# Kernel optimization log

Measured on AMD Instinct MI355X. Metric: run time of the kernel, lower is better.

## Reference

```python
import jax, jax.numpy as jnp
import numpy as np

B, H, W, C = 4, 64, 64, 512
D = C // 8  # query/key channels

def setup_inputs() -> dict:
    key = jax.random.key(0)
    k1, k2, k3, k4, k5 = jax.random.split(key, 5)
    x = jax.random.normal(k1, (B, H, W, C), dtype=jnp.float32)
    # 1x1 convs without bias == per-pixel matmuls; he_normal-ish scaling
    Wq = jax.random.normal(k2, (C, D), dtype=jnp.float32) * np.sqrt(2.0 / C)
    Wk = jax.random.normal(k3, (C, D), dtype=jnp.float32) * np.sqrt(2.0 / C)
    Wv = jax.random.normal(k4, (C, C), dtype=jnp.float32) * np.sqrt(2.0 / C)
    # original init is zeros; use small nonzero so the attention path is exercised
    gamma = jax.random.normal(k5, (1,), dtype=jnp.float32) * 0.1
    return {"x": x, "Wq": Wq, "Wk": Wk, "Wv": Wv, "gamma": gamma}

def reference(x, Wq, Wk, Wv, gamma):
    b, h, w, c = x.shape
    n = h * w
    xf = x.reshape(b, n, c)                      # flatten spatial dims
    q = xf @ Wq                                  # [b, n, c//8]
    k = xf @ Wk                                  # [b, n, c//8]
    v = xf @ Wv                                  # [b, n, c]
    scores = jnp.einsum('bnd,bmd->bnm', q, k)    # [b, n, n]
    attn = jax.nn.sigmoid(scores)                # activation_func='sigmoid' (no row normalization)
    attended = jnp.einsum('bnm,bmc->bnc', attn, v).reshape(b, h, w, c)
    return gamma * attended + x
```

## Files before the change

kernel.cpp:

```cpp
#include <hip/hip_runtime.h>

typedef short bf16x8 __attribute__((ext_vector_type(8)));
typedef float f32x4 __attribute__((ext_vector_type(4)));
typedef unsigned short ushort8v __attribute__((ext_vector_type(8)));
typedef unsigned short ushort4v __attribute__((ext_vector_type(4)));

__device__ __forceinline__ unsigned short f2bf(float f) {
  unsigned u = __float_as_uint(f);
  u += 0x7FFF + ((u >> 16) & 1);
  return (unsigned short)(u >> 16);
}

__global__ void wt_prep(const float* __restrict__ Wq, const float* __restrict__ Wk,
                        const float* __restrict__ Wv, unsigned short* __restrict__ WbT) {
  int idx = blockIdx.x * 256 + threadIdx.x;
  int o = idx >> 9, c = idx & 511;
  float v;
  if (o < 64)       v = Wq[c * 64 + o] * 1.44269504f;
  else if (o < 128) v = Wk[c * 64 + (o - 64)];
  else              v = Wv[(size_t)c * 512 + (o - 128)];
  WbT[idx] = f2bf(v);
}

__global__ __launch_bounds__(256, 2) void proj_gemm(
    const float* __restrict__ x, const unsigned short* __restrict__ WbT,
    unsigned short* __restrict__ q, unsigned short* __restrict__ k,
    unsigned short* __restrict__ vT) {
  __shared__ unsigned short As[128][72];
  const int tid = threadIdx.x;
  const int wid = tid >> 6, lane = tid & 63;
  const int l15 = lane & 15, l4 = lane >> 4;
  const int mtile = blockIdx.x, ntile = blockIdx.y;
  const int rbase = mtile * 128;
  const int wr = (wid >> 1) * 64, wc = (wid & 1) * 64;

  f32x4 acc[4][4] = {};

  const int arow = tid >> 2;
  const int akof = (tid & 3) * 16;

  for (int kb = 0; kb < 512; kb += 64) {
    f32x4 t0[2][4];
#pragma unroll
    for (int pass = 0; pass < 2; ++pass) {
      const float* src = x + (size_t)(rbase + pass * 64 + arow) * 512 + kb + akof;
#pragma unroll
      for (int i = 0; i < 4; ++i) t0[pass][i] = *(const f32x4*)(src + i * 4);
    }
    __syncthreads();
#pragma unroll
    for (int pass = 0; pass < 2; ++pass) {
      unsigned short tmp[16];
#pragma unroll
      for (int i = 0; i < 4; ++i)
#pragma unroll
        for (int j = 0; j < 4; ++j) tmp[i * 4 + j] = f2bf(t0[pass][i][j]);
      unsigned short* dst = &As[pass * 64 + arow][akof];
      *(ushort8v*)(dst)     = *(ushort8v*)(tmp);
      *(ushort8v*)(dst + 8) = *(ushort8v*)(tmp + 8);
    }
    __syncthreads();

    bf16x8 af[4][2], bfr[4][2];
#pragma unroll
    for (int mr = 0; mr < 4; ++mr)
#pragma unroll
      for (int ks = 0; ks < 2; ++ks)
        af[mr][ks] = *(const bf16x8*)&As[wr + mr * 16 + l15][ks * 32 + l4 * 8];
#pragma unroll
    for (int nc = 0; nc < 4; ++nc)
#pragma unroll
      for (int ks = 0; ks < 2; ++ks) {
        int col = ntile * 128 + wc + nc * 16 + l15;
        bfr[nc][ks] = *(const bf16x8*)(WbT + (size_t)col * 512 + kb + ks * 32 + l4 * 8);
      }
#pragma unroll
    for (int ks = 0; ks < 2; ++ks)
#pragma unroll
      for (int mr = 0; mr < 4; ++mr)
#pragma unroll
        for (int nc = 0; nc < 4; ++nc)
          acc[mr][nc] = __builtin_amdgcn_mfma_f32_16x16x32_bf16(af[mr][ks], bfr[nc][ks],
                                                                acc[mr][nc], 0, 0, 0);
  }

  if (ntile == 0) {
    unsigned short* dst = (wid & 1) ? k : q;
#pragma unroll
    for (int mr = 0; mr < 4; ++mr)
#pragma unroll
      for (int nc = 0; nc < 4; ++nc)
#pragma unroll
        for (int r = 0; r < 4; ++r) {
          int grow = rbase + wr + mr * 16 + l4 * 4 + r;
          int col = nc * 16 + l15;
          dst[(size_t)grow * 64 + col] = f2bf(acc[mr][nc][r]);
        }
  } else {
#pragma unroll
    for (int mr = 0; mr < 4; ++mr)
#pragma unroll
      for (int nc = 0; nc < 4; ++nc) {
        int col = ntile * 128 + wc + nc * 16 + l15 - 128;
        int grow = rbase + wr + mr * 16 + l4 * 4;
        int b = grow >> 12, m = grow & 4095;
        ushort4v pk;
#pragma unroll
        for (int r = 0; r < 4; ++r) pk[r] = f2bf(acc[mr][nc][r]);
        *(ushort4v*)(vT + ((size_t)b * 512 + col) * 4096 + m) = pk;
      }
  }
}

__global__ __launch_bounds__(512, 2) void attn_fused(
    const float* __restrict__ x, const unsigned short* __restrict__ q,
    const unsigned short* __restrict__ k, const unsigned short* __restrict__ vT,
    const float* __restrict__ gamma, float* __restrict__ out) {
  __shared__ unsigned short Ks[64][72];
  __shared__ unsigned short Vs[256][72];
  __shared__ unsigned short Ps[128][72];
  const int tid = threadIdx.x, w = tid >> 6, lane = tid & 63;
  const int l15 = lane & 15, l4 = lane >> 4;
  const int rhalf = w >> 2;
  const int mt = w & 3;
  const int rt = blockIdx.x, ct = blockIdx.y, b = blockIdx.z;
  const int rbase = rt * 128, cbase = ct * 256;
  const unsigned short* qb = q + (size_t)b * 4096 * 64;
  const unsigned short* kp = k + (size_t)b * 4096 * 64;
  const unsigned short* vb = vT + (size_t)b * 512 * 4096;
  const float gv = gamma[0];

  const int kst_m = tid >> 3, kst_d = (tid & 7) * 8;
  const int vst_c = tid >> 1, vst_h = (tid & 1) * 32;

  bf16x8 qf[4][2];
#pragma unroll
  for (int rf = 0; rf < 4; ++rf)
#pragma unroll
    for (int ks = 0; ks < 2; ++ks)
      qf[rf][ks] = *(const bf16x8*)(qb +
          (size_t)(rbase + rhalf * 64 + rf * 16 + l15) * 64 + ks * 32 + l4 * 8);

  {
    bf16x8 kreg = *(const bf16x8*)(kp + (size_t)kst_m * 64 + kst_d);
    bf16x8 vreg[4];
#pragma unroll
    for (int i = 0; i < 4; ++i)
      vreg[i] = *(const bf16x8*)(vb + (size_t)(cbase + vst_c) * 4096 + vst_h + i * 8);
    *(bf16x8*)&Ks[kst_m][kst_d] = kreg;
#pragma unroll
    for (int i = 0; i < 4; ++i) *(bf16x8*)&Vs[vst_c][vst_h + i * 8] = vreg[i];
  }
  __syncthreads();

  f32x4 oacc[4][4] = {};

  for (int it = 0; it < 64; ++it) {
    const int mb_n = (it + 1) * 64;
    const bool pf = (it < 63);
    bf16x8 kreg; bf16x8 vreg[4];
    if (pf) {
      kreg = *(const bf16x8*)(kp + (size_t)(mb_n + kst_m) * 64 + kst_d);
#pragma unroll
      for (int i = 0; i < 4; ++i)
        vreg[i] = *(const bf16x8*)(vb + (size_t)(cbase + vst_c) * 4096 + mb_n + vst_h + i * 8);
    }

    f32x4 sacc[4] = {};
#pragma unroll
    for (int ks = 0; ks < 2; ++ks) {
      bf16x8 kf = *(const bf16x8*)&Ks[mt * 16 + l15][ks * 32 + l4 * 8];
#pragma unroll
      for (int rf = 0; rf < 4; ++rf)
        sacc[rf] = __builtin_amdgcn_mfma_f32_16x16x32_bf16(kf, qf[rf][ks], sacc[rf], 0, 0, 0);
    }
#pragma unroll
    for (int rf = 0; rf < 4; ++rf) {
      ushort4v pk;
#pragma unroll
      for (int r = 0; r < 4; ++r) {
        float s = sacc[rf][r];
        pk[r] = f2bf(__builtin_amdgcn_rcpf(1.0f + __builtin_amdgcn_exp2f(-s)));
      }
      *(ushort4v*)&Ps[rhalf * 64 + rf * 16 + l15][mt * 16 + l4 * 4] = pk;
    }
    __syncthreads();

    if (pf) *(bf16x8*)&Ks[kst_m][kst_d] = kreg;

#pragma unroll
    for (int kk = 0; kk < 2; ++kk) {
      bf16x8 af[4], bfr[4];
#pragma unroll
      for (int mr = 0; mr < 4; ++mr)
        af[mr] = *(const bf16x8*)&Ps[rhalf * 64 + mr * 16 + l15][kk * 32 + l4 * 8];
#pragma unroll
      for (int nc = 0; nc < 4; ++nc)
        bfr[nc] = *(const bf16x8*)&Vs[mt * 64 + nc * 16 + l15][kk * 32 + l4 * 8];
#pragma unroll
      for (int mr = 0; mr < 4; ++mr)
#pragma unroll
        for (int nc = 0; nc < 4; ++nc)
          oacc[mr][nc] = __builtin_amdgcn_mfma_f32_16x16x32_bf16(af[mr], bfr[nc],
                                                                 oacc[mr][nc], 0, 0, 0);
    }
    __syncthreads();

    if (pf) {
#pragma unroll
      for (int i = 0; i < 4; ++i) *(bf16x8*)&Vs[vst_c][vst_h + i * 8] = vreg[i];
    }
  }

#pragma unroll
  for (int mr = 0; mr < 4; ++mr)
#pragma unroll
    for (int nc = 0; nc < 4; ++nc)
#pragma unroll
      for (int r = 0; r < 4; ++r) {
        int grow = rbase + rhalf * 64 + mr * 16 + l4 * 4 + r;
        int col = cbase + mt * 64 + nc * 16 + l15;
        size_t idx = ((size_t)b * 4096 + grow) * 512 + col;
        out[idx] = gv * oacc[mr][nc][r] + x[idx];
      }
}

extern "C" void kernel_launch(void* const* d_in, const int* in_sizes, int n_in,
                              void* d_out, int out_size, void* d_ws, size_t ws_size,
                              hipStream_t stream) {
  const float* x     = (const float*)d_in[0];
  const float* Wq    = (const float*)d_in[1];
  const float* Wk    = (const float*)d_in[2];
  const float* Wv    = (const float*)d_in[3];
  const float* gamma = (const float*)d_in[4];
  float* out = (float*)d_out;

  char* ws = (char*)d_ws;
  unsigned short* qbuf = (unsigned short*)(ws);
  unsigned short* kbuf = (unsigned short*)(ws + (2ull << 20));
  unsigned short* vT   = (unsigned short*)(ws + (4ull << 20));
  unsigned short* WbT  = (unsigned short*)(ws + (20ull << 20));

  hipLaunchKernelGGL(wt_prep, dim3(1280), dim3(256), 0, stream, Wq, Wk, Wv, WbT);
  hipLaunchKernelGGL(proj_gemm, dim3(128, 5), dim3(256), 0, stream, x, WbT, qbuf, kbuf, vT);
  hipLaunchKernelGGL(attn_fused, dim3(32, 2, 4), dim3(512), 0, stream,
                     x, qbuf, kbuf, vT, gamma, out);
}
```

Baseline: 162.0 us.

## Shrink attention tile to 64 rows with 256-thread blocks and MFMA priority hints

The attention kernel now processes 64 query rows per block with 4 waves instead of 128 rows with 8 waves, doubling the grid to 512 blocks and redistributing the K/V staging loads per thread. The aim is more blocks for better CU occupancy and load balance. The cost is that each staged K/V tile is reused by half as many rows, which doubles global K/V traffic. s_setprio is also raised around the MFMA sections so matrix work gets issue priority over other waves.

```diff
diff --git a/kernel.cpp b/kernel.cpp
--- a/kernel.cpp
+++ b/kernel.cpp
@@ -112,26 +112,24 @@
   }
 }
 
-__global__ __launch_bounds__(512, 2) void attn_fused(
+__global__ __launch_bounds__(256, 2) void attn_fused(
     const float* __restrict__ x, const unsigned short* __restrict__ q,
     const unsigned short* __restrict__ k, const unsigned short* __restrict__ vT,
     const float* __restrict__ gamma, float* __restrict__ out) {
   __shared__ unsigned short Ks[64][72];
   __shared__ unsigned short Vs[256][72];
-  __shared__ unsigned short Ps[128][72];
+  __shared__ unsigned short Ps[64][72];
   const int tid = threadIdx.x, w = tid >> 6, lane = tid & 63;
   const int l15 = lane & 15, l4 = lane >> 4;
-  const int rhalf = w >> 2;
-  const int mt = w & 3;
   const int rt = blockIdx.x, ct = blockIdx.y, b = blockIdx.z;
-  const int rbase = rt * 128, cbase = ct * 256;
+  const int rbase = rt * 64, cbase = ct * 256;
   const unsigned short* qb = q + (size_t)b * 4096 * 64;
   const unsigned short* kp = k + (size_t)b * 4096 * 64;
   const unsigned short* vb = vT + (size_t)b * 512 * 4096;
   const float gv = gamma[0];
 
-  const int kst_m = tid >> 3, kst_d = (tid & 7) * 8;
-  const int vst_c = tid >> 1, vst_h = (tid & 1) * 32;
+  const int kst_m = tid >> 2, kst_d = (tid & 3) * 16;
+  const int vst_c = tid;
 
   bf16x8 qf[4][2];
 #pragma unroll
@@ -139,17 +137,19 @@
 #pragma unroll
     for (int ks = 0; ks < 2; ++ks)
       qf[rf][ks] = *(const bf16x8*)(qb +
-          (size_t)(rbase + rhalf * 64 + rf * 16 + l15) * 64 + ks * 32 + l4 * 8);
+          (size_t)(rbase + rf * 16 + l15) * 64 + ks * 32 + l4 * 8);
 
   {
-    bf16x8 kreg = *(const bf16x8*)(kp + (size_t)kst_m * 64 + kst_d);
-    bf16x8 vreg[4];
-#pragma unroll
-    for (int i = 0; i < 4; ++i)
-      vreg[i] = *(const bf16x8*)(vb + (size_t)(cbase + vst_c) * 4096 + vst_h + i * 8);
-    *(bf16x8*)&Ks[kst_m][kst_d] = kreg;
-#pragma unroll
-    for (int i = 0; i < 4; ++i) *(bf16x8*)&Vs[vst_c][vst_h + i * 8] = vreg[i];
+    bf16x8 k0 = *(const bf16x8*)(kp + (size_t)kst_m * 64 + kst_d);
+    bf16x8 k1 = *(const bf16x8*)(kp + (size_t)kst_m * 64 + kst_d + 8);
+    bf16x8 vv[8];
+#pragma unroll
+    for (int i = 0; i < 8; ++i)
+      vv[i] = *(const bf16x8*)(vb + (size_t)(cbase + vst_c) * 4096 + i * 8);
+    *(bf16x8*)&Ks[kst_m][kst_d] = k0;
+    *(bf16x8*)&Ks[kst_m][kst_d + 8] = k1;
+#pragma unroll
+    for (int i = 0; i < 8; ++i) *(bf16x8*)&Vs[vst_c][i * 8] = vv[i];
   }
   __syncthreads();
 
@@ -158,22 +158,25 @@
   for (int it = 0; it < 64; ++it) {
     const int mb_n = (it + 1) * 64;
     const bool pf = (it < 63);
-    bf16x8 kreg; bf16x8 vreg[4];
+    bf16x8 k0, k1, vv[8];
     if (pf) {
-      kreg = *(const bf16x8*)(kp + (size_t)(mb_n + kst_m) * 64 + kst_d);
-#pragma unroll
-      for (int i = 0; i < 4; ++i)
-        vreg[i] = *(const bf16x8*)(vb + (size_t)(cbase + vst_c) * 4096 + mb_n + vst_h + i * 8);
+      k0 = *(const bf16x8*)(kp + (size_t)(mb_n + kst_m) * 64 + kst_d);
+      k1 = *(const bf16x8*)(kp + (size_t)(mb_n + kst_m) * 64 + kst_d + 8);
+#pragma unroll
+      for (int i = 0; i < 8; ++i)
+        vv[i] = *(const bf16x8*)(vb + (size_t)(cbase + vst_c) * 4096 + mb_n + i * 8);
     }
 
     f32x4 sacc[4] = {};
+    __builtin_amdgcn_s_setprio(1);
 #pragma unroll
     for (int ks = 0; ks < 2; ++ks) {
-      bf16x8 kf = *(const bf16x8*)&Ks[mt * 16 + l15][ks * 32 + l4 * 8];
+      bf16x8 kf = *(const bf16x8*)&Ks[w * 16 + l15][ks * 32 + l4 * 8];
 #pragma unroll
       for (int rf = 0; rf < 4; ++rf)
         sacc[rf] = __builtin_amdgcn_mfma_f32_16x16x32_bf16(kf, qf[rf][ks], sacc[rf], 0, 0, 0);
     }
+    __builtin_amdgcn_s_setprio(0);
 #pragma unroll
     for (int rf = 0; rf < 4; ++rf) {
       ushort4v pk;
@@ -182,33 +185,38 @@
         float s = sacc[rf][r];
         pk[r] = f2bf(__builtin_amdgcn_rcpf(1.0f + __builtin_amdgcn_exp2f(-s)));
       }
-      *(ushort4v*)&Ps[rhalf * 64 + rf * 16 + l15][mt * 16 + l4 * 4] = pk;
-    }
-    __syncthreads();
-
-    if (pf) *(bf16x8*)&Ks[kst_m][kst_d] = kreg;
+      *(ushort4v*)&Ps[rf * 16 + l15][w * 16 + l4 * 4] = pk;
+    }
+    __syncthreads();
+
+    if (pf) {
+      *(bf16x8*)&Ks[kst_m][kst_d] = k0;
+      *(bf16x8*)&Ks[kst_m][kst_d + 8] = k1;
+    }
 
 #pragma unroll
     for (int kk = 0; kk < 2; ++kk) {
       bf16x8 af[4], bfr[4];
 #pragma unroll
       for (int mr = 0; mr < 4; ++mr)
-        af[mr] = *(const bf16x8*)&Ps[rhalf * 64 + mr * 16 + l15][kk * 32 + l4 * 8];
+        af[mr] = *(const bf16x8*)&Ps[mr * 16 + l15][kk * 32 + l4 * 8];
 #pragma unroll
       for (int nc = 0; nc < 4; ++nc)
-        bfr[nc] = *(const bf16x8*)&Vs[mt * 64 + nc * 16 + l15][kk * 32 + l4 * 8];
+        bfr[nc] = *(const bf16x8*)&Vs[w * 64 + nc * 16 + l15][kk * 32 + l4 * 8];
+      __builtin_amdgcn_s_setprio(1);
 #pragma unroll
       for (int mr = 0; mr < 4; ++mr)
 #pragma unroll
         for (int nc = 0; nc < 4; ++nc)
           oacc[mr][nc] = __builtin_amdgcn_mfma_f32_16x16x32_bf16(af[mr], bfr[nc],
                                                                  oacc[mr][nc], 0, 0, 0);
+      __builtin_amdgcn_s_setprio(0);
     }
     __syncthreads();
 
     if (pf) {
 #pragma unroll
-      for (int i = 0; i < 4; ++i) *(bf16x8*)&Vs[vst_c][vst_h + i * 8] = vreg[i];
+      for (int i = 0; i < 8; ++i) *(bf16x8*)&Vs[vst_c][i * 8] = vv[i];
     }
   }
 
@@ -218,8 +226,8 @@
     for (int nc = 0; nc < 4; ++nc)
 #pragma unroll
       for (int r = 0; r < 4; ++r) {
-        int grow = rbase + rhalf * 64 + mr * 16 + l4 * 4 + r;
-        int col = cbase + mt * 64 + nc * 16 + l15;
+        int grow = rbase + mr * 16 + l4 * 4 + r;
+        int col = cbase + w * 64 + nc * 16 + l15;
         size_t idx = ((size_t)b * 4096 + grow) * 512 + col;
         out[idx] = gv * oacc[mr][nc][r] + x[idx];
       }
@@ -243,6 +251,6 @@
 
   hipLaunchKernelGGL(wt_prep, dim3(1280), dim3(256), 0, stream, Wq, Wk, Wv, WbT);
   hipLaunchKernelGGL(proj_gemm, dim3(128, 5), dim3(256), 0, stream, x, WbT, qbuf, kbuf, vT);
-  hipLaunchKernelGGL(attn_fused, dim3(32, 2, 4), dim3(512), 0, stream,
+  hipLaunchKernelGGL(attn_fused, dim3(64, 2, 4), dim3(256), 0, stream,
                      x, qbuf, kbuf, vT, gamma, out);
 }
```

Measured after the change: 215.9 us. 1.33x slower.

## Double-buffer V and P tiles, keep K in registers, drop a barrier

Applied to the files above, without the earlier changes.

K fragments for the score MFMA are now loaded straight from global memory into registers and prefetched one step ahead, so the K tile no longer passes through LDS. The V tile and the sigmoid probability tile are double-buffered in LDS, which removes the second __syncthreads per iteration. The PV MFMA section is wrapped in s_setprio to favour matrix work. The larger LDS footprint and launch_bounds(512,1) allow only one block per CU, trading occupancy for fewer barriers.

```diff
diff --git a/kernel.cpp b/kernel.cpp
--- a/kernel.cpp
+++ b/kernel.cpp
@@ -112,13 +112,12 @@
   }
 }
 
-__global__ __launch_bounds__(512, 2) void attn_fused(
+__global__ __launch_bounds__(512, 1) void attn_fused(
     const float* __restrict__ x, const unsigned short* __restrict__ q,
     const unsigned short* __restrict__ k, const unsigned short* __restrict__ vT,
     const float* __restrict__ gamma, float* __restrict__ out) {
-  __shared__ unsigned short Ks[64][72];
-  __shared__ unsigned short Vs[256][72];
-  __shared__ unsigned short Ps[128][72];
+  __shared__ unsigned short Vs[2][256][72];
+  __shared__ unsigned short Ps[2][128][72];
   const int tid = threadIdx.x, w = tid >> 6, lane = tid & 63;
   const int l15 = lane & 15, l4 = lane >> 4;
   const int rhalf = w >> 2;
@@ -130,7 +129,6 @@
   const unsigned short* vb = vT + (size_t)b * 512 * 4096;
   const float gv = gamma[0];
 
-  const int kst_m = tid >> 3, kst_d = (tid & 7) * 8;
   const int vst_c = tid >> 1, vst_h = (tid & 1) * 32;
 
   bf16x8 qf[4][2];
@@ -141,39 +139,41 @@
       qf[rf][ks] = *(const bf16x8*)(qb +
           (size_t)(rbase + rhalf * 64 + rf * 16 + l15) * 64 + ks * 32 + l4 * 8);
 
+  bf16x8 kfc[2];
+#pragma unroll
+  for (int ks = 0; ks < 2; ++ks)
+    kfc[ks] = *(const bf16x8*)(kp + (size_t)(mt * 16 + l15) * 64 + ks * 32 + l4 * 8);
   {
-    bf16x8 kreg = *(const bf16x8*)(kp + (size_t)kst_m * 64 + kst_d);
-    bf16x8 vreg[4];
+    bf16x8 vv[4];
 #pragma unroll
     for (int i = 0; i < 4; ++i)
-      vreg[i] = *(const bf16x8*)(vb + (size_t)(cbase + vst_c) * 4096 + vst_h + i * 8);
-    *(bf16x8*)&Ks[kst_m][kst_d] = kreg;
-#pragma unroll
-    for (int i = 0; i < 4; ++i) *(bf16x8*)&Vs[vst_c][vst_h + i * 8] = vreg[i];
-  }
-  __syncthreads();
+      vv[i] = *(const bf16x8*)(vb + (size_t)(cbase + vst_c) * 4096 + vst_h + i * 8);
+#pragma unroll
+    for (int i = 0; i < 4; ++i) *(bf16x8*)&Vs[0][vst_c][vst_h + i * 8] = vv[i];
+  }
 
   f32x4 oacc[4][4] = {};
 
   for (int it = 0; it < 64; ++it) {
     const int mb_n = (it + 1) * 64;
     const bool pf = (it < 63);
-    bf16x8 kreg; bf16x8 vreg[4];
+    const int p = it & 1;
+    bf16x8 kfn[2], vv[4];
     if (pf) {
-      kreg = *(const bf16x8*)(kp + (size_t)(mb_n + kst_m) * 64 + kst_d);
+#pragma unroll
+      for (int ks = 0; ks < 2; ++ks)
+        kfn[ks] = *(const bf16x8*)(kp + (size_t)(mb_n + mt * 16 + l15) * 64 + ks * 32 + l4 * 8);
 #pragma unroll
       for (int i = 0; i < 4; ++i)
-        vreg[i] = *(const bf16x8*)(vb + (size_t)(cbase + vst_c) * 4096 + mb_n + vst_h + i * 8);
+        vv[i] = *(const bf16x8*)(vb + (size_t)(cbase + vst_c) * 4096 + mb_n + vst_h + i * 8);
     }
 
     f32x4 sacc[4] = {};
 #pragma unroll
-    for (int ks = 0; ks < 2; ++ks) {
-      bf16x8 kf = *(const bf16x8*)&Ks[mt * 16 + l15][ks * 32 + l4 * 8];
+    for (int ks = 0; ks < 2; ++ks)
 #pragma unroll
       for (int rf = 0; rf < 4; ++rf)
-        sacc[rf] = __builtin_amdgcn_mfma_f32_16x16x32_bf16(kf, qf[rf][ks], sacc[rf], 0, 0, 0);
-    }
+        sacc[rf] = __builtin_amdgcn_mfma_f32_16x16x32_bf16(kfc[ks], qf[rf][ks], sacc[rf], 0, 0, 0);
 #pragma unroll
     for (int rf = 0; rf < 4; ++rf) {
       ushort4v pk;
@@ -182,21 +182,20 @@
         float s = sacc[rf][r];
         pk[r] = f2bf(__builtin_amdgcn_rcpf(1.0f + __builtin_amdgcn_exp2f(-s)));
       }
-      *(ushort4v*)&Ps[rhalf * 64 + rf * 16 + l15][mt * 16 + l4 * 4] = pk;
+      *(ushort4v*)&Ps[p][rhalf * 64 + rf * 16 + l15][mt * 16 + l4 * 4] = pk;
     }
     __syncthreads();
 
-    if (pf) *(bf16x8*)&Ks[kst_m][kst_d] = kreg;
-
+    __builtin_amdgcn_s_setprio(1);
 #pragma unroll
     for (int kk = 0; kk < 2; ++kk) {
       bf16x8 af[4], bfr[4];
 #pragma unroll
       for (int mr = 0; mr < 4; ++mr)
-        af[mr] = *(const bf16x8*)&Ps[rhalf * 64 + mr * 16 + l15][kk * 32 + l4 * 8];
+        af[mr] = *(const bf16x8*)&Ps[p][rhalf * 64 + mr * 16 + l15][kk * 32 + l4 * 8];
 #pragma unroll
       for (int nc = 0; nc < 4; ++nc)
-        bfr[nc] = *(const bf16x8*)&Vs[mt * 64 + nc * 16 + l15][kk * 32 + l4 * 8];
+        bfr[nc] = *(const bf16x8*)&Vs[p][mt * 64 + nc * 16 + l15][kk * 32 + l4 * 8];
 #pragma unroll
       for (int mr = 0; mr < 4; ++mr)
 #pragma unroll
@@ -204,11 +203,12 @@
           oacc[mr][nc] = __builtin_amdgcn_mfma_f32_16x16x32_bf16(af[mr], bfr[nc],
                                                                  oacc[mr][nc], 0, 0, 0);
     }
-    __syncthreads();
+    __builtin_amdgcn_s_setprio(0);
 
     if (pf) {
 #pragma unroll
-      for (int i = 0; i < 4; ++i) *(bf16x8*)&Vs[vst_c][vst_h + i * 8] = vreg[i];
+      for (int i = 0; i < 4; ++i) *(bf16x8*)&Vs[p ^ 1][vst_c][vst_h + i * 8] = vv[i];
+      kfc[0] = kfn[0]; kfc[1] = kfn[1];
     }
   }
 
```

After: 150.6 us. 7.0% less time.
